# Kernel tuning notes

Measured on AMD Instinct MI355X. Metric: run time of the kernel, lower is better.

## Reference

```python
import jax, jax.numpy as jnp
import numpy as np

B, D_IN, D_H = 16384, 512, 512


def setup_inputs() -> dict:
    key = jax.random.key(0)
    ks = jax.random.split(key, 12)
    scale_w = (2.0 / (D_IN + D_H)) ** 0.5  # xavier-normal-ish
    inp = {
        "X_t": jax.random.normal(ks[0], (B, D_IN), jnp.float32),
        "c_prev": jax.random.normal(ks[1], (B, D_H), jnp.float32),
        "W_f": jax.random.normal(ks[2], (D_IN, D_H), jnp.float32) * scale_w,
        "W_i": jax.random.normal(ks[3], (D_IN, D_H), jnp.float32) * scale_w,
        "W_o": jax.random.normal(ks[4], (D_IN, D_H), jnp.float32) * scale_w,
        "W_c": jax.random.normal(ks[5], (D_IN, D_H), jnp.float32) * scale_w,
        "U_f": jax.random.normal(ks[6], (D_H, D_H), jnp.float32) * (1.0 / D_H ** 0.5),
        "U_i": jax.random.normal(ks[7], (D_H, D_H), jnp.float32) * (1.0 / D_H ** 0.5),
        "U_o": jax.random.normal(ks[8], (D_H, D_H), jnp.float32) * (1.0 / D_H ** 0.5),
        "U_c": jax.random.normal(ks[9], (D_H, D_H), jnp.float32) * (1.0 / D_H ** 0.5),
        "b_f": jnp.zeros((D_H,), jnp.float32),
        "b_i": jnp.zeros((D_H,), jnp.float32),
        "b_o": jnp.zeros((D_H,), jnp.float32),
        "b_c": jnp.zeros((D_H,), jnp.float32),
    }
    return inp


def reference(X_t, c_prev, W_f, W_i, W_o, W_c, U_f, U_i, U_o, U_c, b_f, b_i, b_o, b_c):
    # Fuse the 8 small GEMMs into 2 batched GEMMs (same math: block-concat weights).
    W = jnp.concatenate([W_f, W_i, W_o, W_c], axis=1)  # [D_in, 4H]
    U = jnp.concatenate([U_f, U_i, U_o, U_c], axis=1)  # [H, 4H]
    b = jnp.concatenate([b_f, b_i, b_o, b_c], axis=0)  # [4H]
    pre = X_t @ W + c_prev @ U + b  # [B, 4H]
    f_pre, i_pre, o_pre, c_pre = jnp.split(pre, 4, axis=1)
    f_t = jax.nn.sigmoid(f_pre)
    i_t = jax.nn.sigmoid(i_pre)
    o_t = jax.nn.sigmoid(o_pre)
    c_hat = jnp.tanh(c_pre)
    c_t = f_t * c_prev + i_t * c_hat
    h_t = o_t * jnp.tanh(c_t)
    return h_t
```

## Files before the change

kernel.cpp:

```cpp
#include <hip/hip_runtime.h>

typedef float f32x4 __attribute__((ext_vector_type(4)));
typedef short s16x8 __attribute__((ext_vector_type(8)));
typedef unsigned short u16x8 __attribute__((ext_vector_type(8)));
typedef unsigned int u32;

__device__ __forceinline__ unsigned short f2bf(float f) {
  u32 x = __float_as_uint(f);
  u32 r = (x + 0x7fffu + ((x >> 16) & 1u)) >> 16;
  return (unsigned short)r;
}

__device__ __forceinline__ void gload16(const void* g, void* lds) {
  __builtin_amdgcn_global_load_lds(
      (const __attribute__((address_space(1))) u32*)(uintptr_t)g,
      (__attribute__((address_space(3))) u32*)(u32)(uintptr_t)lds,
      16, 0, 0);
}


__global__ __launch_bounds__(256) void pack_a_kernel(const float* __restrict__ X,
                                                     const float* __restrict__ C,
                                                     unsigned short* __restrict__ At) {
  int idx = blockIdx.x * 256 + threadIdx.x;
  int u = idx >> 10;
  int co = idx & 1023;
  int r = co >> 2, cl = co & 3;
  int bm = u >> 5, ks = (u >> 1) & 15, kh = u & 1;
  int row = bm * 256 + r;
  int kq = cl ^ ((r >> 1) & 3);
  int k = ks * 64 + kh * 32 + kq * 8;
  const float* src = (k < 512) ? (X + (size_t)row * 512 + k)
                               : (C + (size_t)row * 512 + (k - 512));
  float4 v0 = *(const float4*)src;
  float4 v1 = *(const float4*)(src + 4);
  u16x8 h;
  h[0] = f2bf(v0.x); h[1] = f2bf(v0.y); h[2] = f2bf(v0.z); h[3] = f2bf(v0.w);
  h[4] = f2bf(v1.x); h[5] = f2bf(v1.y); h[6] = f2bf(v1.z); h[7] = f2bf(v1.w);
  *(u16x8*)((char*)At + (size_t)idx * 16) = h;
}

__global__ __launch_bounds__(256) void pack_b_kernel(
    const float* __restrict__ Wf, const float* __restrict__ Wi,
    const float* __restrict__ Wo, const float* __restrict__ Wc,
    const float* __restrict__ Uf, const float* __restrict__ Ui,
    const float* __restrict__ Uo, const float* __restrict__ Uc,
    unsigned short* __restrict__ Bt) {
  int idx = blockIdx.x * 256 + threadIdx.x;
  int u = idx >> 10;
  int co = idx & 1023;
  int r = co >> 2, cl = co & 3;
  int bn = u >> 5, ks = (u >> 1) & 15, kh = u & 1;
  int n = bn * 256 + r;
  int g = (n >> 4) & 3;
  int j = ((n >> 6) << 4) | (n & 15);
  int kq = cl ^ ((r >> 1) & 3);
  int k = ks * 64 + kh * 32 + kq * 8;
  const float* Wg = (g == 0) ? Wf : (g == 1) ? Wi : (g == 2) ? Wo : Wc;
  const float* Ug = (g == 0) ? Uf : (g == 1) ? Ui : (g == 2) ? Uo : Uc;
  const float* M = (k < 512) ? (Wg + (size_t)k * 512) : (Ug + (size_t)(k - 512) * 512);
  u16x8 h;
#pragma unroll
  for (int e = 0; e < 8; ++e) h[e] = f2bf(M[(size_t)e * 512 + j]);
  *(u16x8*)((char*)Bt + (size_t)idx * 16) = h;
}


#define BAR    asm volatile("s_barrier" ::: "memory")
#define WAITV8 asm volatile("s_waitcnt vmcnt(8)" ::: "memory")
#define LGKM0  do { asm volatile("s_waitcnt lgkmcnt(0)" ::: "memory"); \
                    __builtin_amdgcn_sched_barrier(0); } while (0)

#define STAGE_A(KS, KH, PDST)                                              \
  do { const char* s_ = gA + (((KS) * 2 + (KH)) << 14) + tid * 16;         \
       char* d_ = lds + (((PDST) * 2 + (KH)) << 14) + tid * 16;            \
       gload16(s_, d_); gload16(s_ + 8192, d_ + 8192); } while (0)
#define STAGE_B(KS, KH, PDST)                                              \
  do { const char* s_ = gB + (((KS) * 2 + (KH)) << 14) + tid * 16;         \
       char* d_ = lds + 65536 + (((PDST) * 2 + (KH)) << 14) + tid * 16;    \
       gload16(s_, d_); gload16(s_ + 8192, d_ + 8192); } while (0)

#define MFMA1(M, N) acc[M][N] = __builtin_amdgcn_mfma_f32_16x16x32_bf16(a##M##_, b##N##_, acc[M][N], 0, 0, 0)

#define PHASE(PAR, KH, MH, STAGE, WAITSTMT)                                          \
  do {                                                                               \
    const char* Ab_ = lds + (((PAR) * 2 + (KH)) << 14) + wr * 8192 + (MH) * 4096;    \
    const char* Bb_ = lds + 65536 + (((PAR) * 2 + (KH)) << 14) + wc * 4096;          \
    s16x8 a0_ = *(const s16x8*)(Ab_ + 0 * 1024 + lsw);                               \
    s16x8 a1_ = *(const s16x8*)(Ab_ + 1 * 1024 + lsw);                               \
    s16x8 a2_ = *(const s16x8*)(Ab_ + 2 * 1024 + lsw);                               \
    s16x8 a3_ = *(const s16x8*)(Ab_ + 3 * 1024 + lsw);                               \
    s16x8 b0_ = *(const s16x8*)(Bb_ + 0 * 1024 + lsw);                               \
    s16x8 b1_ = *(const s16x8*)(Bb_ + 1 * 1024 + lsw);                               \
    s16x8 b2_ = *(const s16x8*)(Bb_ + 2 * 1024 + lsw);                               \
    s16x8 b3_ = *(const s16x8*)(Bb_ + 3 * 1024 + lsw);                               \
    STAGE;                                                                           \
    WAITSTMT;                                                                        \
    BAR;                                                                             \
    LGKM0;                                                                           \
    __builtin_amdgcn_s_setprio(1);                                                   \
    { enum { M0 = (MH) * 4, M1 = M0 + 1, M2 = M0 + 2, M3 = M0 + 3 };                 \
      acc[M0][0] = __builtin_amdgcn_mfma_f32_16x16x32_bf16(a0_, b0_, acc[M0][0],0,0,0); \
      acc[M1][0] = __builtin_amdgcn_mfma_f32_16x16x32_bf16(a1_, b0_, acc[M1][0],0,0,0); \
      acc[M2][0] = __builtin_amdgcn_mfma_f32_16x16x32_bf16(a2_, b0_, acc[M2][0],0,0,0); \
      acc[M3][0] = __builtin_amdgcn_mfma_f32_16x16x32_bf16(a3_, b0_, acc[M3][0],0,0,0); \
      acc[M0][1] = __builtin_amdgcn_mfma_f32_16x16x32_bf16(a0_, b1_, acc[M0][1],0,0,0); \
      acc[M1][1] = __builtin_amdgcn_mfma_f32_16x16x32_bf16(a1_, b1_, acc[M1][1],0,0,0); \
      acc[M2][1] = __builtin_amdgcn_mfma_f32_16x16x32_bf16(a2_, b1_, acc[M2][1],0,0,0); \
      acc[M3][1] = __builtin_amdgcn_mfma_f32_16x16x32_bf16(a3_, b1_, acc[M3][1],0,0,0); \
      acc[M0][2] = __builtin_amdgcn_mfma_f32_16x16x32_bf16(a0_, b2_, acc[M0][2],0,0,0); \
      acc[M1][2] = __builtin_amdgcn_mfma_f32_16x16x32_bf16(a1_, b2_, acc[M1][2],0,0,0); \
      acc[M2][2] = __builtin_amdgcn_mfma_f32_16x16x32_bf16(a2_, b2_, acc[M2][2],0,0,0); \
      acc[M3][2] = __builtin_amdgcn_mfma_f32_16x16x32_bf16(a3_, b2_, acc[M3][2],0,0,0); \
      acc[M0][3] = __builtin_amdgcn_mfma_f32_16x16x32_bf16(a0_, b3_, acc[M0][3],0,0,0); \
      acc[M1][3] = __builtin_amdgcn_mfma_f32_16x16x32_bf16(a1_, b3_, acc[M1][3],0,0,0); \
      acc[M2][3] = __builtin_amdgcn_mfma_f32_16x16x32_bf16(a2_, b3_, acc[M2][3],0,0,0); \
      acc[M3][3] = __builtin_amdgcn_mfma_f32_16x16x32_bf16(a3_, b3_, acc[M3][3],0,0,0); \
    }                                                                                \
    __builtin_amdgcn_s_setprio(0);                                                   \
    __builtin_amdgcn_sched_barrier(0);                                               \
    BAR;                                                                             \
  } while (0)

__global__ __launch_bounds__(512, 2) void gemm_fused(
    const unsigned short* __restrict__ At_, const unsigned short* __restrict__ Bt_,
    const float* __restrict__ c_prev,
    const float* __restrict__ bf_, const float* __restrict__ bi_,
    const float* __restrict__ bo_, const float* __restrict__ bc_,
    float* __restrict__ H) {
  __shared__ __attribute__((aligned(128))) char lds[131072];
  int bid = blockIdx.x;
  int wg = (bid & 7) * 64 + (bid >> 3);
  int bn = wg & 7, bm = wg >> 3;
  int tid = threadIdx.x;
  int lane = tid & 63, w = tid >> 6;
  int wr = w >> 2, wc = w & 3;
  int l15 = lane & 15, kq = lane >> 4;
  int lsw = l15 * 64 + ((kq ^ ((l15 >> 1) & 3)) << 4);

  const char* gA = (const char*)At_ + (size_t)bm * (32 * 16384);
  const char* gB = (const char*)Bt_ + (size_t)bn * (32 * 16384);

  f32x4 acc[8][4] = {};

  STAGE_A(0, 0, 0); STAGE_B(0, 0, 0);
  STAGE_A(0, 1, 0); STAGE_B(0, 1, 0);
  STAGE_A(1, 0, 1); STAGE_B(1, 0, 1);
  WAITV8;
  BAR;

  for (int t = 0; t < 16; t += 2) {
    int p1 = (t + 1) & 15, p2 = (t + 2) & 15, p3 = (t + 3) & 15;
    PHASE(0, 0, 0, STAGE_A(p1, 1, 1), );
    PHASE(0, 0, 1, STAGE_B(p1, 1, 1), WAITV8);
    PHASE(0, 1, 0, STAGE_A(p2, 0, 0), );
    PHASE(0, 1, 1, STAGE_B(p2, 0, 0), WAITV8);
    PHASE(1, 0, 0, STAGE_A(p2, 1, 0), );
    PHASE(1, 0, 1, STAGE_B(p2, 1, 0), WAITV8);
    PHASE(1, 1, 0, STAGE_A(p3, 0, 1), );
    PHASE(1, 1, 1, STAGE_B(p3, 0, 1), WAITV8);
  }

  int j = (bn * 4 + wc) * 16 + l15;
  float vbf = bf_[j], vbi = bi_[j], vbo = bo_[j], vbc = bc_[j];
  int row0 = bm * 256 + wr * 128 + kq * 4;
#pragma unroll
  for (int m = 0; m < 8; ++m) {
#pragma unroll
    for (int ri = 0; ri < 4; ++ri) {
      int row = row0 + m * 16 + ri;
      float fp = acc[m][0][ri] + vbf;
      float ip = acc[m][1][ri] + vbi;
      float op = acc[m][2][ri] + vbo;
      float cq = acc[m][3][ri] + vbc;
      float ft = 1.0f / (1.0f + __expf(-fp));
      float it = 1.0f / (1.0f + __expf(-ip));
      float ot = 1.0f / (1.0f + __expf(-op));
      float ch = 1.0f - 2.0f / (1.0f + __expf(2.0f * cq));
      float cp = c_prev[(size_t)row * 512 + j];
      float ct = ft * cp + it * ch;
      float th = 1.0f - 2.0f / (1.0f + __expf(2.0f * ct));
      H[(size_t)row * 512 + j] = ot * th;
    }
  }
}

extern "C" void kernel_launch(void* const* d_in, const int* in_sizes, int n_in,
                              void* d_out, int out_size, void* d_ws, size_t ws_size,
                              hipStream_t stream) {
  const float* X = (const float*)d_in[0];
  const float* Cp = (const float*)d_in[1];
  const float* Wf = (const float*)d_in[2];
  const float* Wi = (const float*)d_in[3];
  const float* Wo = (const float*)d_in[4];
  const float* Wc = (const float*)d_in[5];
  const float* Uf = (const float*)d_in[6];
  const float* Ui = (const float*)d_in[7];
  const float* Uo = (const float*)d_in[8];
  const float* Uc = (const float*)d_in[9];
  const float* bfp = (const float*)d_in[10];
  const float* bip = (const float*)d_in[11];
  const float* bop = (const float*)d_in[12];
  const float* bcp = (const float*)d_in[13];
  float* H = (float*)d_out;

  unsigned short* At = (unsigned short*)d_ws;
  unsigned short* Bt = (unsigned short*)((char*)d_ws + 33554432u);

  pack_a_kernel<<<8192, 256, 0, stream>>>(X, Cp, At);
  pack_b_kernel<<<1024, 256, 0, stream>>>(Wf, Wi, Wo, Wc, Uf, Ui, Uo, Uc, Bt);
  gemm_fused<<<512, 512, 0, stream>>>(At, Bt, Cp, bfp, bip, bop, bcp, H);
}
```

Before: 100.1 us.

## Software-pipeline LDS fragment loads one phase ahead of MFMAs with double-buffered registers

Each phase now loads the A/B fragments for the next phase from LDS into a second register set, then issues MFMAs on fragments loaded in the previous phase. This removes the explicit lgkmcnt(0) wait in front of each MFMA batch so LDS reads overlap matrix math. The global-load wait threshold is lowered from vmcnt(8) to vmcnt(6) so data is guaranteed resident earlier, which is needed because reads now run one phase ahead. It costs 32 more VGPRs under the 512-thread, 2-block launch bound, which risks spills. The compiler must also insert correct waits for the prefetched registers.

```diff
diff --git a/kernel.cpp b/kernel.cpp
--- a/kernel.cpp
+++ b/kernel.cpp
@@ -68,8 +68,7 @@
 
 #define BAR    asm volatile("s_barrier" ::: "memory")
 #define WAITV8 asm volatile("s_waitcnt vmcnt(8)" ::: "memory")
-#define LGKM0  do { asm volatile("s_waitcnt lgkmcnt(0)" ::: "memory"); \
-                    __builtin_amdgcn_sched_barrier(0); } while (0)
+#define WAITV6 asm volatile("s_waitcnt vmcnt(6)" ::: "memory")
 
 #define STAGE_A(KS, KH, PDST)                                              \
   do { const char* s_ = gA + (((KS) * 2 + (KH)) << 14) + tid * 16;         \
@@ -80,46 +79,52 @@
        char* d_ = lds + 65536 + (((PDST) * 2 + (KH)) << 14) + tid * 16;    \
        gload16(s_, d_); gload16(s_ + 8192, d_ + 8192); } while (0)
 
-#define MFMA1(M, N) acc[M][N] = __builtin_amdgcn_mfma_f32_16x16x32_bf16(a##M##_, b##N##_, acc[M][N], 0, 0, 0)
-
-#define PHASE(PAR, KH, MH, STAGE, WAITSTMT)                                          \
-  do {                                                                               \
-    const char* Ab_ = lds + (((PAR) * 2 + (KH)) << 14) + wr * 8192 + (MH) * 4096;    \
-    const char* Bb_ = lds + 65536 + (((PAR) * 2 + (KH)) << 14) + wc * 4096;          \
-    s16x8 a0_ = *(const s16x8*)(Ab_ + 0 * 1024 + lsw);                               \
-    s16x8 a1_ = *(const s16x8*)(Ab_ + 1 * 1024 + lsw);                               \
-    s16x8 a2_ = *(const s16x8*)(Ab_ + 2 * 1024 + lsw);                               \
-    s16x8 a3_ = *(const s16x8*)(Ab_ + 3 * 1024 + lsw);                               \
-    s16x8 b0_ = *(const s16x8*)(Bb_ + 0 * 1024 + lsw);                               \
-    s16x8 b1_ = *(const s16x8*)(Bb_ + 1 * 1024 + lsw);                               \
-    s16x8 b2_ = *(const s16x8*)(Bb_ + 2 * 1024 + lsw);                               \
-    s16x8 b3_ = *(const s16x8*)(Bb_ + 3 * 1024 + lsw);                               \
-    STAGE;                                                                           \
-    WAITSTMT;                                                                        \
-    BAR;                                                                             \
-    LGKM0;                                                                           \
-    __builtin_amdgcn_s_setprio(1);                                                   \
-    { enum { M0 = (MH) * 4, M1 = M0 + 1, M2 = M0 + 2, M3 = M0 + 3 };                 \
-      acc[M0][0] = __builtin_amdgcn_mfma_f32_16x16x32_bf16(a0_, b0_, acc[M0][0],0,0,0); \
-      acc[M1][0] = __builtin_amdgcn_mfma_f32_16x16x32_bf16(a1_, b0_, acc[M1][0],0,0,0); \
-      acc[M2][0] = __builtin_amdgcn_mfma_f32_16x16x32_bf16(a2_, b0_, acc[M2][0],0,0,0); \
-      acc[M3][0] = __builtin_amdgcn_mfma_f32_16x16x32_bf16(a3_, b0_, acc[M3][0],0,0,0); \
-      acc[M0][1] = __builtin_amdgcn_mfma_f32_16x16x32_bf16(a0_, b1_, acc[M0][1],0,0,0); \
-      acc[M1][1] = __builtin_amdgcn_mfma_f32_16x16x32_bf16(a1_, b1_, acc[M1][1],0,0,0); \
-      acc[M2][1] = __builtin_amdgcn_mfma_f32_16x16x32_bf16(a2_, b1_, acc[M2][1],0,0,0); \
-      acc[M3][1] = __builtin_amdgcn_mfma_f32_16x16x32_bf16(a3_, b1_, acc[M3][1],0,0,0); \
-      acc[M0][2] = __builtin_amdgcn_mfma_f32_16x16x32_bf16(a0_, b2_, acc[M0][2],0,0,0); \
-      acc[M1][2] = __builtin_amdgcn_mfma_f32_16x16x32_bf16(a1_, b2_, acc[M1][2],0,0,0); \
-      acc[M2][2] = __builtin_amdgcn_mfma_f32_16x16x32_bf16(a2_, b2_, acc[M2][2],0,0,0); \
-      acc[M3][2] = __builtin_amdgcn_mfma_f32_16x16x32_bf16(a3_, b2_, acc[M3][2],0,0,0); \
-      acc[M0][3] = __builtin_amdgcn_mfma_f32_16x16x32_bf16(a0_, b3_, acc[M0][3],0,0,0); \
-      acc[M1][3] = __builtin_amdgcn_mfma_f32_16x16x32_bf16(a1_, b3_, acc[M1][3],0,0,0); \
-      acc[M2][3] = __builtin_amdgcn_mfma_f32_16x16x32_bf16(a2_, b3_, acc[M2][3],0,0,0); \
-      acc[M3][3] = __builtin_amdgcn_mfma_f32_16x16x32_bf16(a3_, b3_, acc[M3][3],0,0,0); \
-    }                                                                                \
-    __builtin_amdgcn_s_setprio(0);                                                   \
-    __builtin_amdgcn_sched_barrier(0);                                               \
-    BAR;                                                                             \
+#define LDA4(S, PAR, KH, MH)                                                   \
+  do { const char* p_ = lds + (((PAR) * 2 + (KH)) << 14) + wr * 8192 +         \
+                        (MH) * 4096 + lsw;                                     \
+       S##0 = *(const s16x8*)(p_);                                             \
+       S##1 = *(const s16x8*)(p_ + 1024);                                      \
+       S##2 = *(const s16x8*)(p_ + 2048);                                      \
+       S##3 = *(const s16x8*)(p_ + 3072); } while (0)
+#define LDB4(S, PAR, KH)                                                       \
+  do { const char* p_ = lds + 65536 + (((PAR) * 2 + (KH)) << 14) +             \
+                        wc * 4096 + lsw;                                       \
+       S##0 = *(const s16x8*)(p_);                                             \
+       S##1 = *(const s16x8*)(p_ + 1024);                                      \
+       S##2 = *(const s16x8*)(p_ + 2048);                                      \
+       S##3 = *(const s16x8*)(p_ + 3072); } while (0)
+
+#define MFMA16(M0, A, B)                                                                      \
+  do {                                                                                        \
+    acc[(M0)+0][0] = __builtin_amdgcn_mfma_f32_16x16x32_bf16(A##0, B##0, acc[(M0)+0][0],0,0,0); \
+    acc[(M0)+1][0] = __builtin_amdgcn_mfma_f32_16x16x32_bf16(A##1, B##0, acc[(M0)+1][0],0,0,0); \
+    acc[(M0)+2][0] = __builtin_amdgcn_mfma_f32_16x16x32_bf16(A##2, B##0, acc[(M0)+2][0],0,0,0); \
+    acc[(M0)+3][0] = __builtin_amdgcn_mfma_f32_16x16x32_bf16(A##3, B##0, acc[(M0)+3][0],0,0,0); \
+    acc[(M0)+0][1] = __builtin_amdgcn_mfma_f32_16x16x32_bf16(A##0, B##1, acc[(M0)+0][1],0,0,0); \
+    acc[(M0)+1][1] = __builtin_amdgcn_mfma_f32_16x16x32_bf16(A##1, B##1, acc[(M0)+1][1],0,0,0); \
+    acc[(M0)+2][1] = __builtin_amdgcn_mfma_f32_16x16x32_bf16(A##2, B##1, acc[(M0)+2][1],0,0,0); \
+    acc[(M0)+3][1] = __builtin_amdgcn_mfma_f32_16x16x32_bf16(A##3, B##1, acc[(M0)+3][1],0,0,0); \
+    acc[(M0)+0][2] = __builtin_amdgcn_mfma_f32_16x16x32_bf16(A##0, B##2, acc[(M0)+0][2],0,0,0); \
+    acc[(M0)+1][2] = __builtin_amdgcn_mfma_f32_16x16x32_bf16(A##1, B##2, acc[(M0)+1][2],0,0,0); \
+    acc[(M0)+2][2] = __builtin_amdgcn_mfma_f32_16x16x32_bf16(A##2, B##2, acc[(M0)+2][2],0,0,0); \
+    acc[(M0)+3][2] = __builtin_amdgcn_mfma_f32_16x16x32_bf16(A##3, B##2, acc[(M0)+3][2],0,0,0); \
+    acc[(M0)+0][3] = __builtin_amdgcn_mfma_f32_16x16x32_bf16(A##0, B##3, acc[(M0)+0][3],0,0,0); \
+    acc[(M0)+1][3] = __builtin_amdgcn_mfma_f32_16x16x32_bf16(A##1, B##3, acc[(M0)+1][3],0,0,0); \
+    acc[(M0)+2][3] = __builtin_amdgcn_mfma_f32_16x16x32_bf16(A##2, B##3, acc[(M0)+2][3],0,0,0); \
+    acc[(M0)+3][3] = __builtin_amdgcn_mfma_f32_16x16x32_bf16(A##3, B##3, acc[(M0)+3][3],0,0,0); \
+  } while (0)
+
+#define PHASE(STAGE, WAITSTMT, LOADS, M0, A, B)                                \
+  do {                                                                         \
+    STAGE;                                                                     \
+    WAITSTMT;                                                                  \
+    BAR;                                                                       \
+    LOADS;                                                                     \
+    __builtin_amdgcn_s_setprio(1);                                             \
+    MFMA16(M0, A, B);                                                          \
+    __builtin_amdgcn_s_setprio(0);                                             \
+    __builtin_amdgcn_sched_barrier(0);                                         \
+    BAR;                                                                       \
   } while (0)
 
 __global__ __launch_bounds__(512, 2) void gemm_fused(
@@ -142,23 +147,27 @@
   const char* gB = (const char*)Bt_ + (size_t)bn * (32 * 16384);
 
   f32x4 acc[8][4] = {};
+  s16x8 ap0, ap1, ap2, ap3, aq0, aq1, aq2, aq3;
+  s16x8 bp0, bp1, bp2, bp3, bq0, bq1, bq2, bq3;
 
   STAGE_A(0, 0, 0); STAGE_B(0, 0, 0);
   STAGE_A(0, 1, 0); STAGE_B(0, 1, 0);
   STAGE_A(1, 0, 1); STAGE_B(1, 0, 1);
   WAITV8;
   BAR;
+  LDA4(ap, 0, 0, 0);
+  LDB4(bp, 0, 0);
 
   for (int t = 0; t < 16; t += 2) {
     int p1 = (t + 1) & 15, p2 = (t + 2) & 15, p3 = (t + 3) & 15;
-    PHASE(0, 0, 0, STAGE_A(p1, 1, 1), );
-    PHASE(0, 0, 1, STAGE_B(p1, 1, 1), WAITV8);
-    PHASE(0, 1, 0, STAGE_A(p2, 0, 0), );
-    PHASE(0, 1, 1, STAGE_B(p2, 0, 0), WAITV8);
-    PHASE(1, 0, 0, STAGE_A(p2, 1, 0), );
-    PHASE(1, 0, 1, STAGE_B(p2, 1, 0), WAITV8);
-    PHASE(1, 1, 0, STAGE_A(p3, 0, 1), );
-    PHASE(1, 1, 1, STAGE_B(p3, 0, 1), WAITV8);
+    PHASE(STAGE_A(p1, 1, 1), ,       LDA4(aq, 0, 0, 1),                    0, ap, bp);
+    PHASE(STAGE_B(p1, 1, 1), WAITV6, LDA4(ap, 0, 1, 0); LDB4(bq, 0, 1),   4, aq, bp);
+    PHASE(STAGE_A(p2, 0, 0), ,       LDA4(aq, 0, 1, 1),                    0, ap, bq);
+    PHASE(STAGE_B(p2, 0, 0), WAITV6, LDA4(ap, 1, 0, 0); LDB4(bp, 1, 0),   4, aq, bq);
+    PHASE(STAGE_A(p2, 1, 0), ,       LDA4(aq, 1, 0, 1),                    0, ap, bp);
+    PHASE(STAGE_B(p2, 1, 0), WAITV6, LDA4(ap, 1, 1, 0); LDB4(bq, 1, 1),   4, aq, bp);
+    PHASE(STAGE_A(p3, 0, 1), ,       LDA4(aq, 1, 1, 1),                    0, ap, bq);
+    PHASE(STAGE_B(p3, 0, 1), WAITV6, LDA4(ap, 0, 0, 0); LDB4(bp, 0, 0),   4, aq, bq);
   }
 
   int j = (bn * 4 + wc) * 16 + l15;
```

Result: faster. 97.74 us (-2.3%).
